# Kernel tuning notes

Measured on AMD Instinct MI355X. Metric: run time of the kernel, lower is better.

The kernel has to match this reference:

```python
import jax, jax.numpy as jnp
import numpy as np

N = 50000      # num nodes
E = 800000     # num edges per edge set (before self loops)
F_IN = 256     # encoding_size
F_EMB = 256    # embedding_size
PE = 98        # d2an positional features (beijing)
ALPHA1 = 0.5
ALPHA2 = 0.5


def _uniform_linear(key, out_f, in_f):
    # torch.nn.Linear default init: U(-1/sqrt(in_f), 1/sqrt(in_f))
    s = 1.0 / np.sqrt(in_f)
    return jax.random.uniform(key, (out_f, in_f), jnp.float32, -s, s)


def setup_inputs() -> dict:
    key = jax.random.key(0)
    ks = jax.random.split(key, 18)
    inp = {
        'x': jax.random.normal(ks[0], (N, F_IN), jnp.float32),
        'd2an': jax.random.normal(ks[1], (N, PE), jnp.float32),
        'edge_index_l0': jax.random.randint(ks[2], (2, E), 0, N, jnp.int32),
        'edge_attr_l0': jax.random.uniform(ks[3], (E,), jnp.float32),
        'edge_index_l1': jax.random.randint(ks[4], (2, E), 0, N, jnp.int32),
        'edge_attr_l1': jax.random.uniform(ks[5], (E,), jnp.float32),
        # nodeLin of conv1/conv2 (used only on firstLayer with usePE)
        'Wnode1': _uniform_linear(ks[6], F_IN, F_IN + PE),
        'Wnode2': _uniform_linear(ks[7], F_IN, F_IN + PE),
        # lin1/lin2 of each conv layer (bias-free linears)
        'W11': _uniform_linear(ks[8], F_EMB, F_IN),
        'W12': _uniform_linear(ks[9], F_EMB, F_IN),
        'W21': _uniform_linear(ks[10], F_EMB, F_IN),
        'W22': _uniform_linear(ks[11], F_EMB, F_IN),
        'W31': _uniform_linear(ks[12], F_EMB, F_EMB),
        'W32': _uniform_linear(ks[13], F_EMB, F_EMB),
        'W41': _uniform_linear(ks[14], F_EMB, F_EMB),
        'W42': _uniform_linear(ks[15], F_EMB, F_EMB),
    }
    return inp


def _pos_knn_gnn_layer(x, row, col, attr, d2an, Wnode, W1, W2, first):
    """PosKnnGNNLayer.forward with useSI=True, usePE=True (eval mode).

    message = deg_norm * (x_j @ W1.T) + edge_norm * (x_j @ W2.T), scatter-add to col.
    Linearity lets us aggregate (norm * x_j) first, then apply W1/W2 once per node.
    """
    n = x.shape[0]
    loop = jnp.arange(n, dtype=row.dtype)
    row = jnp.concatenate([row, loop])          # source j
    col = jnp.concatenate([col, loop])          # target i
    attr = jnp.concatenate([attr, jnp.ones((n,), attr.dtype)])  # self-loop weight 1.0

    if first:
        x = jnp.concatenate([x, d2an], axis=1) @ Wnode.T  # [n, F_IN]

    deg = jax.ops.segment_sum(jnp.ones_like(attr), col, num_segments=n)
    dinv = jnp.where(deg > 0, deg ** -0.5, 0.0)
    deg_norm = dinv[row] * dinv[col]            # [E']

    einv = jnp.where(attr > 0, attr ** -0.5, 0.0)
    edge_norm = jnp.minimum(einv, 1.0)          # clamp values > 1.0 to 1.0

    xj = x[row]                                  # gather [E', F]
    a1 = jax.ops.segment_sum(deg_norm[:, None] * xj, col, num_segments=n)
    a2 = jax.ops.segment_sum(edge_norm[:, None] * xj, col, num_segments=n)
    return a1 @ W1.T + a2 @ W2.T                 # [n, F_EMB]


def reference(x, d2an, edge_index_l0, edge_attr_l0, edge_index_l1, edge_attr_l1,
              Wnode1, Wnode2, W11, W12, W21, W22, W31, W32, W41, W42):
    r0, c0 = edge_index_l0[0], edge_index_l0[1]
    r1, c1 = edge_index_l1[0], edge_index_l1[1]

    x0 = jax.nn.relu(_pos_knn_gnn_layer(x, r0, c0, edge_attr_l0, d2an, Wnode1, W11, W12, True))
    x1 = jax.nn.relu(_pos_knn_gnn_layer(x, r1, c1, edge_attr_l1, d2an, Wnode2, W21, W22, True))
    h = ALPHA1 * x0 + ALPHA2 * x1               # dropout p=0.3 is identity in eval

    x0 = jax.nn.relu(_pos_knn_gnn_layer(h, r0, c0, edge_attr_l0, None, None, W31, W32, False))
    x1 = jax.nn.relu(_pos_knn_gnn_layer(h, r1, c1, edge_attr_l1, None, None, W41, W42, False))
    return ALPHA1 * x0 + ALPHA2 * x1
```

## Files before the change

kernel.cpp:

```cpp
#include <hip/hip_runtime.h>


using bf16x8  = __attribute__((ext_vector_type(8))) __bf16;
using floatx4 = __attribute__((ext_vector_type(4))) float;

__device__ __forceinline__ float b2f(unsigned short b) {
    return __uint_as_float(((unsigned)b) << 16);
}
__device__ __forceinline__ unsigned short f2b(float f) {
    unsigned u = __float_as_uint(f);
    return (unsigned short)((u + 0x7FFFu + ((u >> 16) & 1u)) >> 16);
}
__device__ __forceinline__ unsigned short f2h(float f) {
    _Float16 h = (_Float16)f;
    return __builtin_bit_cast(unsigned short, h);
}
__device__ __forceinline__ float h2f(unsigned short u) {
    return (float)__builtin_bit_cast(_Float16, u);
}


__global__ void k_cnt2(const int* __restrict__ col0, const int* __restrict__ col1,
                       int E, int* __restrict__ cnt0, int* __restrict__ cnt1) {
    int e = blockIdx.x * 256 + threadIdx.x;
    const int* col = blockIdx.y ? col1 : col0;
    int* cnt = blockIdx.y ? cnt1 : cnt0;
    if (e < E) atomicAdd(&cnt[col[e]], 1);
}

__global__ __launch_bounds__(1024) void k_scan2(
    const int* __restrict__ cnt0, const int* __restrict__ cnt1,
    int* __restrict__ off0, int* __restrict__ off1, int n) {
    const int* cnt = blockIdx.y ? cnt1 : cnt0;
    int* off = blockIdx.y ? off1 : off0;
    __shared__ int wsum[16];
    __shared__ int wpre[16];
    __shared__ int carry;
    const int t = threadIdx.x;
    const int lane = t & 63;
    const int w = t >> 6;
    if (t == 0) { carry = 0; off[0] = 0; }
    __syncthreads();
    for (int base = 0; base < n; base += 1024) {
        int i = base + t;
        int v = (i < n) ? ((cnt[i] + 7) & ~7) : 0;
        #pragma unroll
        for (int d = 1; d < 64; d <<= 1) {
            int u = __shfl_up(v, d, 64);
            if (lane >= d) v += u;
        }
        if (lane == 63) wsum[w] = v;
        __syncthreads();
        if (t < 16) {
            int s = wsum[t];
            #pragma unroll
            for (int d = 1; d < 16; d <<= 1) {
                int u = __shfl_up(s, d, 16);
                if (t >= d) s += u;
            }
            wpre[t] = s;
        }
        __syncthreads();
        int add = carry + (w > 0 ? wpre[w - 1] : 0);
        if (i < n) off[i + 1] = v + add;
        __syncthreads();
        if (t == 0) carry += wpre[15];
        __syncthreads();
    }
}

__global__ void k_prep(const int* __restrict__ cnt0, const int* __restrict__ cnt1,
                       const int* __restrict__ off0, const int* __restrict__ off1,
                       float* __restrict__ dinv0, float* __restrict__ dinv1,
                       int* __restrict__ cur0, int* __restrict__ cur1, int n) {
    int i = blockIdx.x * 256 + threadIdx.x;
    if (i >= n) return;
    const int* cnt = blockIdx.y ? cnt1 : cnt0;
    const int* off = blockIdx.y ? off1 : off0;
    float* dinv = blockIdx.y ? dinv1 : dinv0;
    int* cur = blockIdx.y ? cur1 : cur0;
    dinv[i] = rsqrtf((float)(cnt[i] + 1));
    cur[i] = off[i];
}

__global__ void k_fill2(const int* __restrict__ ei0, const float* __restrict__ ea0,
                        const int* __restrict__ ei1, const float* __restrict__ ea1,
                        int E, const float* __restrict__ dinv0,
                        const float* __restrict__ dinv1,
                        int* __restrict__ cur0, int* __restrict__ cur1,
                        uint2* __restrict__ rec0, uint2* __restrict__ rec1) {
    int e = blockIdx.x * 256 + threadIdx.x;
    if (e >= E) return;
    const int* ei = blockIdx.y ? ei1 : ei0;
    const float* ea = blockIdx.y ? ea1 : ea0;
    const float* dinv = blockIdx.y ? dinv1 : dinv0;
    int* cur = blockIdx.y ? cur1 : cur0;
    uint2* rec = blockIdx.y ? rec1 : rec0;
    int r = ei[e];
    int c = ei[E + e];
    float a = ea[e];
    float w2 = (a > 0.0f) ? fminf(rsqrtf(a), 1.0f) : 0.0f;
    float w1 = dinv[r] * dinv[c];
    int p = atomicAdd(&cur[c], 1);
    rec[p] = make_uint2((unsigned)r,
                        ((unsigned)f2h(w1) << 16) | (unsigned)f2h(w2));
}

__global__ void k_pad(const int* __restrict__ cnt0, const int* __restrict__ cnt1,
                      const int* __restrict__ off0, const int* __restrict__ off1,
                      uint2* __restrict__ rec0, uint2* __restrict__ rec1, int n) {
    int i = blockIdx.x * 256 + threadIdx.x;
    if (i >= n) return;
    const int* cnt = blockIdx.y ? cnt1 : cnt0;
    const int* off = blockIdx.y ? off1 : off0;
    uint2* rec = blockIdx.y ? rec1 : rec0;
    int p = off[i] + cnt[i], pe = off[i + 1];
    for (; p < pe; ++p) rec[p] = make_uint2(0u, 0u);
}


__global__ void k_xc(const float* __restrict__ x, const float* __restrict__ pe,
                     unsigned short* __restrict__ xc, int n, int F, int PEd,
                     int KC, int KP) {
    int idx = blockIdx.x * 256 + threadIdx.x;
    if (idx >= n * KP) return;
    int i = idx / KP, k = idx - i * KP;
    float v = 0.0f;
    if (k < F)        v = x[(size_t)i * F + k];
    else if (k < KC)  v = pe[(size_t)i * PEd + (k - F)];
    xc[idx] = f2b(v);
}

__global__ void k_wall(const float* __restrict__ Wn1, const float* __restrict__ Wn2,
                       const float* __restrict__ W11, const float* __restrict__ W12,
                       const float* __restrict__ W21, const float* __restrict__ W22,
                       const float* __restrict__ W31, const float* __restrict__ W32,
                       const float* __restrict__ W41, const float* __restrict__ W42,
                       unsigned short* __restrict__ wn0c, unsigned short* __restrict__ wn1c,
                       unsigned short* __restrict__ wc0, unsigned short* __restrict__ wc1,
                       unsigned short* __restrict__ wc2, unsigned short* __restrict__ wc3,
                       int F, int KC, int KP) {
    int idx = blockIdx.x * 256 + threadIdx.x;
    int npad = F * KP;
    if (idx < 2 * npad) {
        const float* W = (idx < npad) ? Wn1 : Wn2;
        unsigned short* Wc = (idx < npad) ? wn0c : wn1c;
        int t = (idx < npad) ? idx : idx - npad;
        int o = t / KP, k = t - o * KP;
        Wc[t] = f2b(k < KC ? W[(size_t)o * KC + k] : 0.0f);
        return;
    }
    int t = idx - 2 * npad;
    int seg = F * 512;
    if (t >= 4 * seg) return;
    int which = t / seg;
    int r = t - which * seg;
    const float* Wa = (which == 0) ? W11 : (which == 1) ? W21 : (which == 2) ? W31 : W41;
    const float* Wb = (which == 0) ? W12 : (which == 1) ? W22 : (which == 2) ? W32 : W42;
    unsigned short* Wc = (which == 0) ? wc0 : (which == 1) ? wc1 : (which == 2) ? wc2 : wc3;
    int o = r >> 9, k = r & 511;
    float v = (k < 256) ? Wa[(size_t)o * 256 + k] : Wb[(size_t)o * 256 + (k - 256)];
    Wc[r] = f2b(v);
}

__global__ __launch_bounds__(256) void k_agg(
    const unsigned short* __restrict__ X0, const unsigned short* __restrict__ X1,
    const int* __restrict__ off0, const int* __restrict__ off1,
    const uint2* __restrict__ rec0, const uint2* __restrict__ rec1,
    const float* __restrict__ dinv0, const float* __restrict__ dinv1,
    unsigned short* __restrict__ A0, unsigned short* __restrict__ A1, int n) {
    const int s = blockIdx.y;
    const unsigned short* X = s ? X1 : X0;
    const int* off = s ? off1 : off0;
    const uint2* rec = s ? rec1 : rec0;
    const float* dinv = s ? dinv1 : dinv0;
    unsigned short* A = s ? A1 : A0;

    const int gw = (blockIdx.x * 256 + threadIdx.x) >> 6;
    const int lane = threadIdx.x & 63;
    if (gw >= n) return;

    const int e0 = __builtin_amdgcn_readfirstlane(off[gw]);
    const int e1 = __builtin_amdgcn_readfirstlane(off[gw + 1]);
    const float di = dinv[gw];
    const uint2* X2 = (const uint2*)X;
    uint2 xs = X2[(size_t)gw * 64 + lane];

    float acc1[4] = {0.f, 0.f, 0.f, 0.f};
    float acc2[4] = {0.f, 0.f, 0.f, 0.f};

    for (int base = e0; base < e1; base += 8) {
        uint2 rr[8];
        #pragma unroll
        for (int k = 0; k < 8; k++) rr[k] = rec[base + k];
        uint2 g[8];
        #pragma unroll
        for (int k = 0; k < 8; k++) {
            unsigned src = (unsigned)__builtin_amdgcn_readfirstlane(rr[k].x);
            g[k] = X2[(size_t)src * 64 + lane];
        }
        #pragma unroll
        for (int k = 0; k < 8; k++) {
            float w1 = h2f((unsigned short)(rr[k].y >> 16));
            float w2 = h2f((unsigned short)(rr[k].y & 0xFFFFu));
            float v0 = __uint_as_float(g[k].x << 16);
            float v1 = __uint_as_float(g[k].x & 0xFFFF0000u);
            float v2 = __uint_as_float(g[k].y << 16);
            float v3 = __uint_as_float(g[k].y & 0xFFFF0000u);
            acc1[0] += w1 * v0; acc1[1] += w1 * v1; acc1[2] += w1 * v2; acc1[3] += w1 * v3;
            acc2[0] += w2 * v0; acc2[1] += w2 * v1; acc2[2] += w2 * v2; acc2[3] += w2 * v3;
        }
    }

    {
        float v0 = __uint_as_float(xs.x << 16);
        float v1 = __uint_as_float(xs.x & 0xFFFF0000u);
        float v2 = __uint_as_float(xs.y << 16);
        float v3 = __uint_as_float(xs.y & 0xFFFF0000u);
        float ws = di * di;
        acc1[0] += ws * v0; acc1[1] += ws * v1; acc1[2] += ws * v2; acc1[3] += ws * v3;
        acc2[0] += v0;      acc2[1] += v1;      acc2[2] += v2;      acc2[3] += v3;
    }

    uint2 o1, o2;
    o1.x = (unsigned)f2b(acc1[0]) | ((unsigned)f2b(acc1[1]) << 16);
    o1.y = (unsigned)f2b(acc1[2]) | ((unsigned)f2b(acc1[3]) << 16);
    o2.x = (unsigned)f2b(acc2[0]) | ((unsigned)f2b(acc2[1]) << 16);
    o2.y = (unsigned)f2b(acc2[2]) | ((unsigned)f2b(acc2[3]) << 16);
    *(uint2*)(A + (size_t)gw * 512 + lane * 4) = o1;
    *(uint2*)(A + (size_t)gw * 512 + 256 + lane * 4) = o2;
}

#define GLL(g, l) \
    __builtin_amdgcn_global_load_lds((__attribute__((address_space(1))) void*)(g), \
                                     (__attribute__((address_space(3))) void*)(l), 16, 0, 0)

__global__ __launch_bounds__(256) void gemm_bt(
    const unsigned short* __restrict__ A,
    const unsigned short* __restrict__ B0, const unsigned short* __restrict__ B1,
    int M, int K, int Nc,
    unsigned short* __restrict__ outH0, unsigned short* __restrict__ outH1) {
    const unsigned short* B = blockIdx.z ? B1 : B0;
    unsigned short* outH = blockIdx.z ? outH1 : outH0;

    __shared__ __align__(16) unsigned short sA[128 * 32];
    __shared__ __align__(16) unsigned short sB[128 * 32];
    const int tid = threadIdx.x;
    const int lane = tid & 63;
    const int wave = tid >> 6;
    const int bm = blockIdx.x * 128;
    const int bn = blockIdx.y * 128;

    const int r0 = wave * 32 + (lane >> 2);
    const int kcol = (lane & 3) * 8;
    const int ga0 = min(bm + r0, M - 1);
    const int ga1 = min(bm + r0 + 16, M - 1);
    const int gb0 = min(bn + r0, Nc - 1);
    const int gb1 = min(bn + r0 + 16, Nc - 1);
    const unsigned short* pa0 = A + (size_t)ga0 * K + kcol;
    const unsigned short* pa1 = A + (size_t)ga1 * K + kcol;
    const unsigned short* pb0 = B + (size_t)gb0 * K + kcol;
    const unsigned short* pb1 = B + (size_t)gb1 * K + kcol;
    unsigned short* la0 = &sA[wave * 1024];
    unsigned short* la1 = &sA[wave * 1024 + 512];
    unsigned short* lb0 = &sB[wave * 1024];
    unsigned short* lb1 = &sB[wave * 1024 + 512];

    floatx4 acc[4][4];
    #pragma unroll
    for (int i = 0; i < 4; i++)
        #pragma unroll
        for (int j = 0; j < 4; j++) acc[i][j] = (floatx4){0.f, 0.f, 0.f, 0.f};

    const int mbase = (wave & 1) * 64 + (lane & 15);
    const int nbase = (wave >> 1) * 64 + (lane & 15);
    const int koff = (lane >> 4) * 8;

    for (int kk = 0; kk < K; kk += 32) {
        GLL(pa0 + kk, la0);
        GLL(pa1 + kk, la1);
        GLL(pb0 + kk, lb0);
        GLL(pb1 + kk, lb1);
        __syncthreads();
        bf16x8 af[4], bf[4];
        #pragma unroll
        for (int mi = 0; mi < 4; mi++)
            af[mi] = *(const bf16x8*)&sA[(mbase + mi * 16) * 32 + koff];
        #pragma unroll
        for (int ni = 0; ni < 4; ni++)
            bf[ni] = *(const bf16x8*)&sB[(nbase + ni * 16) * 32 + koff];
        #pragma unroll
        for (int mi = 0; mi < 4; mi++)
            #pragma unroll
            for (int ni = 0; ni < 4; ni++)
                acc[mi][ni] = __builtin_amdgcn_mfma_f32_16x16x32_bf16(
                    af[mi], bf[ni], acc[mi][ni], 0, 0, 0);
        __syncthreads();
    }

    const int crow = bm + (wave & 1) * 64 + (lane >> 4) * 4;
    const int ccol = bn + (wave >> 1) * 64 + (lane & 15);
    #pragma unroll
    for (int mi = 0; mi < 4; mi++)
        #pragma unroll
        for (int ni = 0; ni < 4; ni++)
            #pragma unroll
            for (int r = 0; r < 4; r++) {
                int row = crow + mi * 16 + r;
                if (row >= M) continue;
                int col = ccol + ni * 16;
                outH[(size_t)row * Nc + col] = f2b(acc[mi][ni][r]);
            }
}

__global__ __launch_bounds__(256) void gemm_dual(
    const unsigned short* __restrict__ A0, const unsigned short* __restrict__ B0,
    const unsigned short* __restrict__ A1, const unsigned short* __restrict__ B1,
    int M, int K, int Nc,
    float* __restrict__ outF, unsigned short* __restrict__ outH, float alpha) {
    __shared__ __align__(16) unsigned short sA[128 * 32];
    __shared__ __align__(16) unsigned short sB[128 * 32];
    const int tid = threadIdx.x;
    const int lane = tid & 63;
    const int wave = tid >> 6;
    const int bm = blockIdx.x * 128;
    const int bn = blockIdx.y * 128;

    const int r0 = wave * 32 + (lane >> 2);
    const int kcol = (lane & 3) * 8;
    const int ga0 = min(bm + r0, M - 1);
    const int ga1 = min(bm + r0 + 16, M - 1);
    const int gb0 = min(bn + r0, Nc - 1);
    const int gb1 = min(bn + r0 + 16, Nc - 1);
    unsigned short* la0 = &sA[wave * 1024];
    unsigned short* la1 = &sA[wave * 1024 + 512];
    unsigned short* lb0 = &sB[wave * 1024];
    unsigned short* lb1 = &sB[wave * 1024 + 512];

    const int mbase = (wave & 1) * 64 + (lane & 15);
    const int nbase = (wave >> 1) * 64 + (lane & 15);
    const int koff = (lane >> 4) * 8;

    floatx4 acc[4][4], res[4][4];

    #pragma unroll
    for (int pass = 0; pass < 2; pass++) {
        const unsigned short* A = pass ? A1 : A0;
        const unsigned short* B = pass ? B1 : B0;
        const unsigned short* pa0 = A + (size_t)ga0 * K + kcol;
        const unsigned short* pa1 = A + (size_t)ga1 * K + kcol;
        const unsigned short* pb0 = B + (size_t)gb0 * K + kcol;
        const unsigned short* pb1 = B + (size_t)gb1 * K + kcol;
        #pragma unroll
        for (int i = 0; i < 4; i++)
            #pragma unroll
            for (int j = 0; j < 4; j++) acc[i][j] = (floatx4){0.f, 0.f, 0.f, 0.f};

        for (int kk = 0; kk < K; kk += 32) {
            GLL(pa0 + kk, la0);
            GLL(pa1 + kk, la1);
            GLL(pb0 + kk, lb0);
            GLL(pb1 + kk, lb1);
            __syncthreads();
            bf16x8 af[4], bf[4];
            #pragma unroll
            for (int mi = 0; mi < 4; mi++)
                af[mi] = *(const bf16x8*)&sA[(mbase + mi * 16) * 32 + koff];
            #pragma unroll
            for (int ni = 0; ni < 4; ni++)
                bf[ni] = *(const bf16x8*)&sB[(nbase + ni * 16) * 32 + koff];
            #pragma unroll
            for (int mi = 0; mi < 4; mi++)
                #pragma unroll
                for (int ni = 0; ni < 4; ni++)
                    acc[mi][ni] = __builtin_amdgcn_mfma_f32_16x16x32_bf16(
                        af[mi], bf[ni], acc[mi][ni], 0, 0, 0);
            __syncthreads();
        }
        if (pass == 0) {
            #pragma unroll
            for (int mi = 0; mi < 4; mi++)
                #pragma unroll
                for (int ni = 0; ni < 4; ni++)
                    #pragma unroll
                    for (int r = 0; r < 4; r++)
                        res[mi][ni][r] = fmaxf(acc[mi][ni][r], 0.0f);
        }
    }

    const int crow = bm + (wave & 1) * 64 + (lane >> 4) * 4;
    const int ccol = bn + (wave >> 1) * 64 + (lane & 15);
    #pragma unroll
    for (int mi = 0; mi < 4; mi++)
        #pragma unroll
        for (int ni = 0; ni < 4; ni++)
            #pragma unroll
            for (int r = 0; r < 4; r++) {
                int row = crow + mi * 16 + r;
                if (row >= M) continue;
                int col = ccol + ni * 16;
                float v = alpha * (res[mi][ni][r] + fmaxf(acc[mi][ni][r], 0.0f));
                size_t idx = (size_t)row * Nc + col;
                if (outF) outF[idx] = v;
                else      outH[idx] = f2b(v);
            }
}


extern "C" void kernel_launch(void* const* d_in, const int* in_sizes, int n_in,
                              void* d_out, int out_size, void* d_ws, size_t ws_size,
                              hipStream_t stream) {
    const int F = 256;
    const int N = in_sizes[0] / F;
    const int PEd = in_sizes[1] / N;
    const int E = in_sizes[2] / 2;
    const int KC = F + PEd;
    const int KP = (KC + 31) & ~31;

    const float* x   = (const float*)d_in[0];
    const float* pe  = (const float*)d_in[1];
    const int*   ei0 = (const int*)d_in[2];
    const float* ea0 = (const float*)d_in[3];
    const int*   ei1 = (const int*)d_in[4];
    const float* ea1 = (const float*)d_in[5];
    const float* Wn1 = (const float*)d_in[6];
    const float* Wn2 = (const float*)d_in[7];
    const float* W11 = (const float*)d_in[8];
    const float* W12 = (const float*)d_in[9];
    const float* W21 = (const float*)d_in[10];
    const float* W22 = (const float*)d_in[11];
    const float* W31 = (const float*)d_in[12];
    const float* W32 = (const float*)d_in[13];
    const float* W41 = (const float*)d_in[14];
    const float* W42 = (const float*)d_in[15];
    float* out = (float*)d_out;

    char* p = (char*)d_ws;
    auto alloc = [&](size_t b) -> char* {
        char* r = p;
        p += (b + 255) & ~(size_t)255;
        return r;
    };
    int*   cnt0  = (int*)alloc((size_t)N * 4);
    int*   cnt1  = (int*)alloc((size_t)N * 4);
    int*   off0  = (int*)alloc((size_t)(N + 1) * 4);
    int*   off1  = (int*)alloc((size_t)(N + 1) * 4);
    int*   cur0  = (int*)alloc((size_t)N * 4);
    int*   cur1  = (int*)alloc((size_t)N * 4);
    float* dinv0 = (float*)alloc((size_t)N * 4);
    float* dinv1 = (float*)alloc((size_t)N * 4);
    uint2* rec0  = (uint2*)alloc(((size_t)E + 8ull * N) * 8);
    uint2* rec1  = (uint2*)alloc(((size_t)E + 8ull * N) * 8);
    unsigned short* wn0c = (unsigned short*)alloc((size_t)F * KP * 2);
    unsigned short* wn1c = (unsigned short*)alloc((size_t)F * KP * 2);
    unsigned short* wc0  = (unsigned short*)alloc((size_t)F * 512 * 2);
    unsigned short* wc1  = (unsigned short*)alloc((size_t)F * 512 * 2);
    unsigned short* wc2  = (unsigned short*)alloc((size_t)F * 512 * 2);
    unsigned short* wc3  = (unsigned short*)alloc((size_t)F * 512 * 2);
    unsigned short* xa   = (unsigned short*)alloc((size_t)N * 512 * 2);
    unsigned short* xb   = xa + (size_t)N * 256;
    unsigned short* h    = (unsigned short*)alloc((size_t)N * F * 2);
    unsigned short* a12  = (unsigned short*)alloc((size_t)N * 512 * 2);
    unsigned short* xc   = a12;
    unsigned short* a12bL1 = (unsigned short*)d_out;
    unsigned short* a12bL2 = xa;

    const int B = 256;
    const int gE = (E + B - 1) / B;
    const int gN = (N + B - 1) / B;
    const int gW = (N + 3) / 4;
    dim3 gemm_grid((N + 127) / 128, 2);
    dim3 gemm_grid2((N + 127) / 128, 2, 2);

    hipMemsetAsync(cnt0, 0, (size_t)N * 4, stream);
    hipMemsetAsync(cnt1, 0, (size_t)N * 4, stream);
    k_cnt2<<<dim3(gE, 2), B, 0, stream>>>(ei0 + E, ei1 + E, E, cnt0, cnt1);
    k_scan2<<<dim3(1, 2), 1024, 0, stream>>>(cnt0, cnt1, off0, off1, N);
    k_prep<<<dim3(gN, 2), B, 0, stream>>>(cnt0, cnt1, off0, off1, dinv0, dinv1, cur0, cur1, N);
    k_fill2<<<dim3(gE, 2), B, 0, stream>>>(ei0, ea0, ei1, ea1, E, dinv0, dinv1,
                                           cur0, cur1, rec0, rec1);
    k_pad<<<dim3(gN, 2), B, 0, stream>>>(cnt0, cnt1, off0, off1, rec0, rec1, N);

    k_xc<<<((size_t)N * KP + B - 1) / B, B, 0, stream>>>(x, pe, xc, N, F, PEd, KC, KP);
    {
        int tot = 2 * F * KP + 4 * F * 512;
        k_wall<<<(tot + B - 1) / B, B, 0, stream>>>(Wn1, Wn2, W11, W12, W21, W22,
                                                    W31, W32, W41, W42,
                                                    wn0c, wn1c, wc0, wc1, wc2, wc3,
                                                    F, KC, KP);
    }

    gemm_bt<<<gemm_grid2, B, 0, stream>>>(xc, wn0c, wn1c, N, KP, F, xa, xb);

    k_agg<<<dim3(gW, 2), B, 0, stream>>>(xa, xb, off0, off1, rec0, rec1,
                                         dinv0, dinv1, a12, a12bL1, N);
    gemm_dual<<<gemm_grid, B, 0, stream>>>(a12, wc0, a12bL1, wc1, N, 512, F,
                                           nullptr, h, 0.5f);

    k_agg<<<dim3(gW, 2), B, 0, stream>>>(h, h, off0, off1, rec0, rec1,
                                         dinv0, dinv1, a12, a12bL2, N);
    gemm_dual<<<gemm_grid, B, 0, stream>>>(a12, wc2, a12bL2, wc3, N, 512, F,
                                           out, nullptr, 0.5f);
}
```

Before: 783.7 us.

## Parallelize CSR offset scan and widen aggregation gathers to half-wave row reads

The single-block serial prefix scan becomes a three-kernel multi-block scan (per-block scan, scan of block sums, add-back). The self loop is now written into the padded edge records with weights dinv^2 and 1.0, so the aggregation kernel no longer reads dinv or does a separate self term. Aggregation now has each half-wave gather a full 512-byte row with 16-byte loads, handling two edges per wave step. It accumulates with packed FMAs and combines the halves with a cross-lane shuffle. This cuts the number of load instructions per edge and the serial scan latency, at the cost of extra launches and a shuffle reduction.

```diff
diff --git a/kernel.cpp b/kernel.cpp
--- a/kernel.cpp
+++ b/kernel.cpp
@@ -3,6 +3,7 @@
 
 using bf16x8  = __attribute__((ext_vector_type(8))) __bf16;
 using floatx4 = __attribute__((ext_vector_type(4))) float;
+using f32x2   = __attribute__((ext_vector_type(2))) float;
 
 __device__ __forceinline__ float b2f(unsigned short b) {
     return __uint_as_float(((unsigned)b) << 16);
@@ -28,45 +29,63 @@
     if (e < E) atomicAdd(&cnt[col[e]], 1);
 }
 
-__global__ __launch_bounds__(1024) void k_scan2(
+__global__ __launch_bounds__(1024) void k_scanA(
     const int* __restrict__ cnt0, const int* __restrict__ cnt1,
-    int* __restrict__ off0, int* __restrict__ off1, int n) {
+    int* __restrict__ off0, int* __restrict__ off1,
+    int* __restrict__ bs0, int* __restrict__ bs1, int n) {
     const int* cnt = blockIdx.y ? cnt1 : cnt0;
     int* off = blockIdx.y ? off1 : off0;
+    int* bs  = blockIdx.y ? bs1 : bs0;
     __shared__ int wsum[16];
     __shared__ int wpre[16];
-    __shared__ int carry;
     const int t = threadIdx.x;
     const int lane = t & 63;
     const int w = t >> 6;
-    if (t == 0) { carry = 0; off[0] = 0; }
+    const int i = blockIdx.x * 1024 + t;
+    int v = (i < n) ? ((cnt[i] + 8) & ~7) : 0;
+    #pragma unroll
+    for (int d = 1; d < 64; d <<= 1) {
+        int u = __shfl_up(v, d, 64);
+        if (lane >= d) v += u;
+    }
+    if (lane == 63) wsum[w] = v;
     __syncthreads();
-    for (int base = 0; base < n; base += 1024) {
-        int i = base + t;
-        int v = (i < n) ? ((cnt[i] + 7) & ~7) : 0;
-        #pragma unroll
-        for (int d = 1; d < 64; d <<= 1) {
-            int u = __shfl_up(v, d, 64);
-            if (lane >= d) v += u;
+    if (t < 16) {
+        int s2 = wsum[t];
+        #pragma unroll
+        for (int d = 1; d < 16; d <<= 1) {
+            int u = __shfl_up(s2, d, 16);
+            if (t >= d) s2 += u;
         }
-        if (lane == 63) wsum[w] = v;
-        __syncthreads();
-        if (t < 16) {
-            int s = wsum[t];
-            #pragma unroll
-            for (int d = 1; d < 16; d <<= 1) {
-                int u = __shfl_up(s, d, 16);
-                if (t >= d) s += u;
-            }
-            wpre[t] = s;
-        }
-        __syncthreads();
-        int add = carry + (w > 0 ? wpre[w - 1] : 0);
-        if (i < n) off[i + 1] = v + add;
-        __syncthreads();
-        if (t == 0) carry += wpre[15];
-        __syncthreads();
-    }
+        wpre[t] = s2;
+    }
+    __syncthreads();
+    int incl = v + (w > 0 ? wpre[w - 1] : 0);
+    if (i < n) off[i + 1] = incl;
+    if (t == 1023) bs[blockIdx.x] = incl;
+}
+
+__global__ void k_scanB(int* __restrict__ bs0, int* __restrict__ bs1, int nb) {
+    int* bs = blockIdx.y ? bs1 : bs0;
+    const int t = threadIdx.x;
+    int v = (t < nb) ? bs[t] : 0;
+    int orig = v;
+    #pragma unroll
+    for (int d = 1; d < 64; d <<= 1) {
+        int u = __shfl_up(v, d, 64);
+        if (t >= d) v += u;
+    }
+    if (t < nb) bs[t] = v - orig;
+}
+
+__global__ __launch_bounds__(1024) void k_scanC(
+    const int* __restrict__ bs0, const int* __restrict__ bs1,
+    int* __restrict__ off0, int* __restrict__ off1, int n) {
+    int* off = blockIdx.y ? off1 : off0;
+    const int* bs = blockIdx.y ? bs1 : bs0;
+    const int i = blockIdx.x * 1024 + threadIdx.x;
+    if (i == 0) off[0] = 0;
+    if (i < n && blockIdx.x > 0) off[i + 1] += bs[blockIdx.x];
 }
 
 __global__ void k_prep(const int* __restrict__ cnt0, const int* __restrict__ cnt1,
@@ -108,13 +127,18 @@
 
 __global__ void k_pad(const int* __restrict__ cnt0, const int* __restrict__ cnt1,
                       const int* __restrict__ off0, const int* __restrict__ off1,
+                      const float* __restrict__ dinv0, const float* __restrict__ dinv1,
                       uint2* __restrict__ rec0, uint2* __restrict__ rec1, int n) {
     int i = blockIdx.x * 256 + threadIdx.x;
     if (i >= n) return;
     const int* cnt = blockIdx.y ? cnt1 : cnt0;
     const int* off = blockIdx.y ? off1 : off0;
+    const float* dinv = blockIdx.y ? dinv1 : dinv0;
     uint2* rec = blockIdx.y ? rec1 : rec0;
     int p = off[i] + cnt[i], pe = off[i + 1];
+    float di = dinv[i];
+    rec[p++] = make_uint2((unsigned)i,
+                          ((unsigned)f2h(di * di) << 16) | 0x3C00u);
     for (; p < pe; ++p) rec[p] = make_uint2(0u, 0u);
 }
 
@@ -167,13 +191,11 @@
     const unsigned short* __restrict__ X0, const unsigned short* __restrict__ X1,
     const int* __restrict__ off0, const int* __restrict__ off1,
     const uint2* __restrict__ rec0, const uint2* __restrict__ rec1,
-    const float* __restrict__ dinv0, const float* __restrict__ dinv1,
     unsigned short* __restrict__ A0, unsigned short* __restrict__ A1, int n) {
     const int s = blockIdx.y;
-    const unsigned short* X = s ? X1 : X0;
+    const char* Xb = (const char*)(s ? X1 : X0);
     const int* off = s ? off1 : off0;
     const uint2* rec = s ? rec1 : rec0;
-    const float* dinv = s ? dinv1 : dinv0;
     unsigned short* A = s ? A1 : A0;
 
     const int gw = (blockIdx.x * 256 + threadIdx.x) >> 6;
@@ -182,53 +204,70 @@
 
     const int e0 = __builtin_amdgcn_readfirstlane(off[gw]);
     const int e1 = __builtin_amdgcn_readfirstlane(off[gw + 1]);
-    const float di = dinv[gw];
-    const uint2* X2 = (const uint2*)X;
-    uint2 xs = X2[(size_t)gw * 64 + lane];
-
-    float acc1[4] = {0.f, 0.f, 0.f, 0.f};
-    float acc2[4] = {0.f, 0.f, 0.f, 0.f};
-
-    for (int base = e0; base < e1; base += 8) {
-        uint2 rr[8];
-        #pragma unroll
-        for (int k = 0; k < 8; k++) rr[k] = rec[base + k];
-        uint2 g[8];
-        #pragma unroll
-        for (int k = 0; k < 8; k++) {
-            unsigned src = (unsigned)__builtin_amdgcn_readfirstlane(rr[k].x);
-            g[k] = X2[(size_t)src * 64 + lane];
+    const bool hi = lane >= 32;
+    const unsigned loff = (unsigned)(lane & 31) << 4;
+
+    f32x2 acc1[4], acc2[4];
+    #pragma unroll
+    for (int d = 0; d < 4; ++d) {
+        acc1[d] = (f32x2){0.f, 0.f};
+        acc2[d] = (f32x2){0.f, 0.f};
+    }
+
+    const uint4* recq = (const uint4*)(rec + e0);
+    const int nit = (e1 - e0) >> 3;
+    for (int it = 0; it < nit; ++it) {
+        uint4 q[4];
+        #pragma unroll
+        for (int k = 0; k < 4; ++k) q[k] = recq[it * 4 + k];
+        uint4 g[4];
+        unsigned wsel[4];
+        #pragma unroll
+        for (int k = 0; k < 4; ++k) {
+            unsigned srcsel = hi ? q[k].z : q[k].x;
+            wsel[k] = hi ? q[k].w : q[k].y;
+            g[k] = *(const uint4*)(Xb + (((srcsel << 9) | loff)));
         }
         #pragma unroll
-        for (int k = 0; k < 8; k++) {
-            float w1 = h2f((unsigned short)(rr[k].y >> 16));
-            float w2 = h2f((unsigned short)(rr[k].y & 0xFFFFu));
-            float v0 = __uint_as_float(g[k].x << 16);
-            float v1 = __uint_as_float(g[k].x & 0xFFFF0000u);
-            float v2 = __uint_as_float(g[k].y << 16);
-            float v3 = __uint_as_float(g[k].y & 0xFFFF0000u);
-            acc1[0] += w1 * v0; acc1[1] += w1 * v1; acc1[2] += w1 * v2; acc1[3] += w1 * v3;
-            acc2[0] += w2 * v0; acc2[1] += w2 * v1; acc2[2] += w2 * v2; acc2[3] += w2 * v3;
+        for (int k = 0; k < 4; ++k) {
+            float w1 = h2f((unsigned short)(wsel[k] >> 16));
+            float w2 = h2f((unsigned short)(wsel[k] & 0xFFFFu));
+            f32x2 w1v = {w1, w1};
+            f32x2 w2v = {w2, w2};
+            const unsigned* gd = (const unsigned*)&g[k];
+            #pragma unroll
+            for (int d = 0; d < 4; ++d) {
+                f32x2 v;
+                v.x = __uint_as_float(gd[d] << 16);
+                v.y = __uint_as_float(gd[d] & 0xFFFF0000u);
+                acc1[d] = __builtin_elementwise_fma(w1v, v, acc1[d]);
+                acc2[d] = __builtin_elementwise_fma(w2v, v, acc2[d]);
+            }
         }
     }
 
-    {
-        float v0 = __uint_as_float(xs.x << 16);
-        float v1 = __uint_as_float(xs.x & 0xFFFF0000u);
-        float v2 = __uint_as_float(xs.y << 16);
-        float v3 = __uint_as_float(xs.y & 0xFFFF0000u);
-        float ws = di * di;
-        acc1[0] += ws * v0; acc1[1] += ws * v1; acc1[2] += ws * v2; acc1[3] += ws * v3;
-        acc2[0] += v0;      acc2[1] += v1;      acc2[2] += v2;      acc2[3] += v3;
-    }
-
-    uint2 o1, o2;
-    o1.x = (unsigned)f2b(acc1[0]) | ((unsigned)f2b(acc1[1]) << 16);
-    o1.y = (unsigned)f2b(acc1[2]) | ((unsigned)f2b(acc1[3]) << 16);
-    o2.x = (unsigned)f2b(acc2[0]) | ((unsigned)f2b(acc2[1]) << 16);
-    o2.y = (unsigned)f2b(acc2[2]) | ((unsigned)f2b(acc2[3]) << 16);
-    *(uint2*)(A + (size_t)gw * 512 + lane * 4) = o1;
-    *(uint2*)(A + (size_t)gw * 512 + 256 + lane * 4) = o2;
+    float o1[8], o2[8];
+    #pragma unroll
+    for (int d = 0; d < 4; ++d) {
+        o1[2 * d]     = acc1[d].x + __shfl_xor(acc1[d].x, 32);
+        o1[2 * d + 1] = acc1[d].y + __shfl_xor(acc1[d].y, 32);
+        o2[2 * d]     = acc2[d].x + __shfl_xor(acc2[d].x, 32);
+        o2[2 * d + 1] = acc2[d].y + __shfl_xor(acc2[d].y, 32);
+    }
+    float s0 = hi ? o2[0] : o1[0];
+    float s1 = hi ? o2[1] : o1[1];
+    float s2 = hi ? o2[2] : o1[2];
+    float s3 = hi ? o2[3] : o1[3];
+    float s4 = hi ? o2[4] : o1[4];
+    float s5 = hi ? o2[5] : o1[5];
+    float s6 = hi ? o2[6] : o1[6];
+    float s7 = hi ? o2[7] : o1[7];
+    uint4 o;
+    o.x = (unsigned)f2b(s0) | ((unsigned)f2b(s1) << 16);
+    o.y = (unsigned)f2b(s2) | ((unsigned)f2b(s3) << 16);
+    o.z = (unsigned)f2b(s4) | ((unsigned)f2b(s5) << 16);
+    o.w = (unsigned)f2b(s6) | ((unsigned)f2b(s7) << 16);
+    *(uint4*)(A + (size_t)gw * 512 + (hi ? 256 : 0) + ((lane & 31) << 3)) = o;
 }
 
 #define GLL(g, l) \
@@ -449,6 +488,8 @@
     int*   cur1  = (int*)alloc((size_t)N * 4);
     float* dinv0 = (float*)alloc((size_t)N * 4);
     float* dinv1 = (float*)alloc((size_t)N * 4);
+    int*   bs0   = (int*)alloc(64 * 4);
+    int*   bs1   = (int*)alloc(64 * 4);
     uint2* rec0  = (uint2*)alloc(((size_t)E + 8ull * N) * 8);
     uint2* rec1  = (uint2*)alloc(((size_t)E + 8ull * N) * 8);
     unsigned short* wn0c = (unsigned short*)alloc((size_t)F * KP * 2);
@@ -469,17 +510,21 @@
     const int gE = (E + B - 1) / B;
     const int gN = (N + B - 1) / B;
     const int gW = (N + 3) / 4;
+    const int nb = (N + 1023) / 1024;
     dim3 gemm_grid((N + 127) / 128, 2);
     dim3 gemm_grid2((N + 127) / 128, 2, 2);
 
     hipMemsetAsync(cnt0, 0, (size_t)N * 4, stream);
     hipMemsetAsync(cnt1, 0, (size_t)N * 4, stream);
     k_cnt2<<<dim3(gE, 2), B, 0, stream>>>(ei0 + E, ei1 + E, E, cnt0, cnt1);
-    k_scan2<<<dim3(1, 2), 1024, 0, stream>>>(cnt0, cnt1, off0, off1, N);
+    k_scanA<<<dim3(nb, 2), 1024, 0, stream>>>(cnt0, cnt1, off0, off1, bs0, bs1, N);
+    k_scanB<<<dim3(1, 2), 64, 0, stream>>>(bs0, bs1, nb);
+    k_scanC<<<dim3(nb, 2), 1024, 0, stream>>>(bs0, bs1, off0, off1, N);
     k_prep<<<dim3(gN, 2), B, 0, stream>>>(cnt0, cnt1, off0, off1, dinv0, dinv1, cur0, cur1, N);
     k_fill2<<<dim3(gE, 2), B, 0, stream>>>(ei0, ea0, ei1, ea1, E, dinv0, dinv1,
                                            cur0, cur1, rec0, rec1);
-    k_pad<<<dim3(gN, 2), B, 0, stream>>>(cnt0, cnt1, off0, off1, rec0, rec1, N);
+    k_pad<<<dim3(gN, 2), B, 0, stream>>>(cnt0, cnt1, off0, off1, dinv0, dinv1,
+                                         rec0, rec1, N);
 
     k_xc<<<((size_t)N * KP + B - 1) / B, B, 0, stream>>>(x, pe, xc, N, F, PEd, KC, KP);
     {
@@ -493,12 +538,12 @@
     gemm_bt<<<gemm_grid2, B, 0, stream>>>(xc, wn0c, wn1c, N, KP, F, xa, xb);
 
     k_agg<<<dim3(gW, 2), B, 0, stream>>>(xa, xb, off0, off1, rec0, rec1,
-                                         dinv0, dinv1, a12, a12bL1, N);
+                                         a12, a12bL1, N);
     gemm_dual<<<gemm_grid, B, 0, stream>>>(a12, wc0, a12bL1, wc1, N, 512, F,
                                            nullptr, h, 0.5f);
 
     k_agg<<<dim3(gW, 2), B, 0, stream>>>(h, h, off0, off1, rec0, rec1,
-                                         dinv0, dinv1, a12, a12bL2, N);
+                                         a12, a12bL2, N);
     gemm_dual<<<gemm_grid, B, 0, stream>>>(a12, wc2, a12bL2, wc3, N, 512, F,
                                            out, nullptr, 0.5f);
 }
```

Result: slower. 924.2 us (+17.9%).
